# Kernel optimization log

Hardware: AMD Instinct MI355X
Metric: run time of the kernel (lower is better)

Reference implementation:

```python
import jax, jax.numpy as jnp
import numpy as np

C = 256
HEADS = 8
HD = C // HEADS
SCALE = HD ** -0.5


def conv1x1(x, W, b):
    # x: [B,C_in,H,W], W: [C_out,C_in], b: [C_out]
    return jnp.einsum('oc,bchw->bohw', W, x) + b[None, :, None, None]


def setup_inputs() -> dict:
    key = jax.random.key(0)
    ks = jax.random.split(key, 12)
    B, H, Wd = 2, 48, 48
    s = C ** -0.5
    return {
        'x': jax.random.normal(ks[0], (B, C, H, Wd), jnp.float32),
        'uncertainty': jax.random.uniform(ks[1], (B, 1, H, Wd), jnp.float32),
        'Wq': jax.random.normal(ks[2], (C, C), jnp.float32) * s,
        'bq': jnp.zeros((C,), jnp.float32),
        'Wk': jax.random.normal(ks[3], (C, C), jnp.float32) * s,
        'bk': jnp.zeros((C,), jnp.float32),
        'Wv': jax.random.normal(ks[4], (C, C), jnp.float32) * s,
        'bv': jnp.zeros((C,), jnp.float32),
        'Wg': jax.random.normal(ks[5], (C, 1), jnp.float32),
        'bg': jnp.zeros((C,), jnp.float32),
        'Wo': jax.random.normal(ks[6], (C, C), jnp.float32) * s,
        'bo': jnp.zeros((C,), jnp.float32),
    }


def reference(x, uncertainty, Wq, bq, Wk, bk, Wv, bv, Wg, bg, Wo, bo):
    B, _, H, Wd = x.shape
    N = H * Wd
    # uncertainty gate (1x1 conv from 1 channel to C channels)
    uw = conv1x1(uncertainty, Wg, bg)            # [B,C,H,W]
    gated_x = x * (1.0 - uw)
    q = conv1x1(gated_x, Wq, bq).reshape(B, HEADS, HD, N)
    k = conv1x1(gated_x, Wk, bk).reshape(B, HEADS, HD, N)
    v = conv1x1(x, Wv, bv).reshape(B, HEADS, HD, N)
    # scores: [B,h,N,N] (query tokens n, key tokens m)
    scores = jnp.einsum('bhdn,bhdm->bhnm', q, k) * SCALE
    u_flat = uncertainty.reshape(B, 1, 1, N)      # mask over key axis
    scores = scores * (1.0 - u_flat)
    attn = jax.nn.softmax(scores, axis=-1)
    out = jnp.einsum('bhnm,bhdm->bhdn', attn, v)  # [B,h,hd,N]
    out = out.reshape(B, C, H, Wd)
    out = conv1x1(out, Wo, bo)
    return out + x
```

## Files before the change

kernel.cpp:

```cpp
#include <hip/hip_runtime.h>
#include <hip/hip_bf16.h>

typedef float f32x4 __attribute__((ext_vector_type(4)));
typedef __bf16 bf16x8 __attribute__((ext_vector_type(8)));
typedef __bf16 bf16x4 __attribute__((ext_vector_type(4)));
typedef short s16x4 __attribute__((ext_vector_type(4)));

constexpr int C = 256;
constexpr int N = 2304;
constexpr int T = 2 * N;

#if __has_builtin(__builtin_amdgcn_exp2f)
#define EXP2F(x) __builtin_amdgcn_exp2f(x)
#else
#define EXP2F(x) exp2f(x)
#endif

__device__ __forceinline__ bf16x8 load_bf8(const __bf16* p) {
    return *reinterpret_cast<const bf16x8*>(p);
}

__device__ __forceinline__ f32x4 mfma32(bf16x8 a, bf16x8 b, f32x4 c) {
    return __builtin_amdgcn_mfma_f32_16x16x32_bf16(a, b, c, 0, 0, 0);
}

#if __has_builtin(__builtin_amdgcn_mfma_f32_16x16x16bf16_1k)
__device__ __forceinline__ f32x4 mfma16(bf16x4 a, bf16x4 b, f32x4 c) {
    return __builtin_amdgcn_mfma_f32_16x16x16bf16_1k(
        __builtin_bit_cast(s16x4, a), __builtin_bit_cast(s16x4, b), c, 0, 0, 0);
}
#else
__device__ __forceinline__ f32x4 mfma16(bf16x4 a, bf16x4 b, f32x4 c) {
    f32x4 d;
    asm volatile("v_mfma_f32_16x16x16_bf16 %0, %1, %2, %3"
                 : "=v"(d) : "v"(a), "v"(b), "v"(c));
    return d;
}
#endif

__device__ __forceinline__ void gload_lds16(const __bf16* g, __bf16* l) {
    __builtin_amdgcn_global_load_lds(
        (const __attribute__((address_space(1))) void*)g,
        (__attribute__((address_space(3))) void*)l, 16, 0, 0);
}

#define VMCNT2() asm volatile("s_waitcnt vmcnt(2)" ::: "memory")
#define VMCNT0() asm volatile("s_waitcnt vmcnt(0)" ::: "memory")
#define LGKM0()  asm volatile("s_waitcnt lgkmcnt(0)" ::: "memory")

__global__ void prep_kernel(const float* __restrict__ x, const float* __restrict__ u,
                            const float* __restrict__ Wg, const float* __restrict__ bg,
                            const float* __restrict__ Wq, const float* __restrict__ Wk,
                            const float* __restrict__ Wv, const float* __restrict__ Wo,
                            __bf16* __restrict__ xT, __bf16* __restrict__ gxT,
                            __bf16* __restrict__ Wb) {
    __shared__ float tile[32][65];
    int t = threadIdx.x;
    if (blockIdx.x >= 576) {
        int u2 = blockIdx.x - 576;
        const float* srcs[4] = {Wq, Wk, Wv, Wo};
        int m = u2 >> 6;
        int idx = (u2 & 63) * 256 + t;
        float4 v = reinterpret_cast<const float4*>(srcs[m])[idx];
        bf16x4 o = { (__bf16)v.x, (__bf16)v.y, (__bf16)v.z, (__bf16)v.w };
        reinterpret_cast<bf16x4*>(Wb + m * 65536)[idx] = o;
        return;
    }
    int uu = blockIdx.x;
    int n0 = (uu % 36) * 64;
    int c0 = ((uu / 36) & 7) * 32;
    int b = uu / 288;
    const float* xp = x + (b * C + c0) * N + n0;
    #pragma unroll
    for (int rr = 0; rr < 8; ++rr) {
        int cl = rr * 4 + (t >> 6);
        int nl = t & 63;
        tile[cl][nl] = xp[cl * N + nl];
    }
    __syncthreads();
    int cq = (t & 7) * 4;
    #pragma unroll
    for (int it = 0; it < 2; ++it) {
        int nl = it * 32 + (t >> 3);
        float uv = u[b * N + n0 + nl];
        bf16x4 xo, go;
        #pragma unroll
        for (int jj = 0; jj < 4; ++jj) {
            int cch = c0 + cq + jj;
            float xv = tile[cq + jj][nl];
            float gate = 1.0f - (Wg[cch] * uv + bg[cch]);
            xo[jj] = (__bf16)xv;
            go[jj] = (__bf16)(xv * gate);
        }
        int tok = b * N + n0 + nl;
        *reinterpret_cast<bf16x4*>(xT + (long)tok * C + c0 + cq) = xo;
        *reinterpret_cast<bf16x4*>(gxT + (long)tok * C + c0 + cq) = go;
    }
}

__global__ __launch_bounds__(256) void qkv_kernel(const __bf16* __restrict__ Wb,
    const __bf16* __restrict__ xT, const __bf16* __restrict__ gxT,
    const float* __restrict__ bq, const float* __restrict__ bk, const float* __restrict__ bv,
    const float* __restrict__ u,
    __bf16* __restrict__ Q, __bf16* __restrict__ K, __bf16* __restrict__ V) {
    int L = blockIdx.x;
    int h = L & 7;
    int rest = L >> 3;
    int c = rest % 36;
    int z = rest / 36;
    int wave = threadIdx.x >> 6, lane = threadIdx.x & 63;
    int g = lane >> 4, r = lane & 15;
    int ow = h * 32 + (wave & 1) * 16;
    int t0 = c * 128 + (wave >> 1) * 64;
    const __bf16* W = Wb + z * 65536;
    const __bf16* inp = (z == 2) ? xT : gxT;
    f32x4 acc[4] = {};
    for (int k = 0; k < 8; ++k) {
        bf16x8 a = load_bf8(W + (ow + r) * C + k * 32 + g * 8);
        #pragma unroll
        for (int tb = 0; tb < 4; ++tb) {
            bf16x8 bfr = load_bf8(inp + (long)(t0 + tb * 16 + r) * C + k * 32 + g * 8);
            acc[tb] = mfma32(a, bfr, acc[tb]);
        }
    }
    const float* bias = (z == 0) ? bq : (z == 1) ? bk : bv;
    float bvw[4];
    #pragma unroll
    for (int i = 0; i < 4; ++i) bvw[i] = bias[ow + g * 4 + i];
    int d0 = (wave & 1) * 16 + g * 4;
    const float SC = 0.17677669529663687f * 1.4426950408889634f;
    #pragma unroll
    for (int tb = 0; tb < 4; ++tb) {
        int t = t0 + tb * 16 + r;
        int b = t / N, n = t % N;
        if (z == 2) {
            #pragma unroll
            for (int i = 0; i < 4; ++i)
                V[((long)(b * 8 + h) * 32 + d0 + i) * N + n] = (__bf16)(acc[tb][i] + bvw[i]);
        } else {
            bf16x4 outv;
            if (z == 1) {
                float scale = SC * (1.0f - u[t]);
                #pragma unroll
                for (int i = 0; i < 4; ++i) outv[i] = (__bf16)((acc[tb][i] + bvw[i]) * scale);
            } else {
                #pragma unroll
                for (int i = 0; i < 4; ++i) outv[i] = (__bf16)(acc[tb][i] + bvw[i]);
            }
            __bf16* dst = (z == 0) ? Q : K;
            *reinterpret_cast<bf16x4*>(dst + ((long)(b * 8 + h) * N + n) * 32 + d0) = outv;
        }
    }
}

__global__ __launch_bounds__(512) void attn_kernel(const __bf16* __restrict__ Q,
    const __bf16* __restrict__ K, const __bf16* __restrict__ V,
    __bf16* __restrict__ aoT) {
    __shared__ __bf16 sMem[16384];
    int id = blockIdx.x;
    int xcd = id & 7, j = id >> 3;
    int bh = xcd + 8 * (j / 36);
    int qblk = j % 36;
    int tid = threadIdx.x;
    int wave = tid >> 6, lane = tid & 63;
    int grp = wave >> 2, wv = wave & 3;
    int g = lane >> 4, r = lane & 15;
    int q0w = qblk * 64 + wv * 16;
    const __bf16* Qg = Q + (long)bh * N * 32;
    const __bf16* Kg = K + (long)bh * N * 32 + (long)grp * 1152 * 32;
    const __bf16* Vg = V + (long)bh * 32 * N + grp * 1152;
    bf16x8 qf = load_bf8(Qg + (q0w + r) * 32 + g * 8);
    int s_ = (wv << 6) | lane;
    int l_ = s_ ^ ((s_ >> 3) & 7);
    const __bf16* kS = Kg + (l_ >> 2) * 32 + (l_ & 3) * 8;
    const __bf16* vS = Vg + (long)(l_ >> 3) * N + (l_ & 7) * 8;
    __bf16* kB = sMem + grp * 8192;
    __bf16* vB = kB + 4096;
    int so = wv * 512;
    auto STAGE = [&](long m0, int buf) {
        gload_lds16(kS + m0 * 32, kB + buf * 2048 + so);
        gload_lds16(vS + m0,      vB + buf * 2048 + so);
    };
    int pk[4], pv[4][2];
    #pragma unroll
    for (int t = 0; t < 4; ++t) {
        int ck = (t * 16 + r) * 4 + g;
        pk[t] = (ck ^ ((ck >> 3) & 7)) * 8;
        #pragma unroll
        for (int dt = 0; dt < 2; ++dt) {
            int cv = (dt * 16 + r) * 8 + t * 2 + (g >> 1);
            pv[t][dt] = (cv ^ ((cv >> 3) & 7)) * 8 + (g & 1) * 4;
        }
    }
    bf16x4 onesv;
    #pragma unroll
    for (int i = 0; i < 4; ++i) onesv[i] = (__bf16)1.0f;
    f32x4 oa0 = {}, oa1 = {}, oal = {};
    STAGE(0, 0);
    STAGE(64, 1);
    for (int t = 0; t < 18; ++t) {
        if (t < 17) { VMCNT2(); } else { VMCNT0(); }
        __builtin_amdgcn_s_barrier();
        const __bf16* kb = kB + (t & 1) * 2048;
        const __bf16* vb = vB + (t & 1) * 2048;
        bf16x8 kc0 = load_bf8(kb + pk[0]);
        bf16x8 kc1 = load_bf8(kb + pk[1]);
        bf16x8 kc2 = load_bf8(kb + pk[2]);
        bf16x8 kc3 = load_bf8(kb + pk[3]);
        bf16x4 vf[4][2];
        #pragma unroll
        for (int tt = 0; tt < 4; ++tt)
            #pragma unroll
            for (int dt = 0; dt < 2; ++dt)
                vf[tt][dt] = *reinterpret_cast<const bf16x4*>(vb + pv[tt][dt]);
        f32x4 z = {};
        __builtin_amdgcn_s_setprio(1);
        f32x4 s0 = mfma32(kc0, qf, z);
        f32x4 s1 = mfma32(kc1, qf, z);
        f32x4 s2 = mfma32(kc2, qf, z);
        f32x4 s3 = mfma32(kc3, qf, z);
        __builtin_amdgcn_s_setprio(0);
        bf16x4 pa0, pa1, pa2, pa3;
        #pragma unroll
        for (int i = 0; i < 4; ++i) pa0[i] = (__bf16)EXP2F(s0[i]);
        #pragma unroll
        for (int i = 0; i < 4; ++i) pa1[i] = (__bf16)EXP2F(s1[i]);
        #pragma unroll
        for (int i = 0; i < 4; ++i) pa2[i] = (__bf16)EXP2F(s2[i]);
        #pragma unroll
        for (int i = 0; i < 4; ++i) pa3[i] = (__bf16)EXP2F(s3[i]);
        __builtin_amdgcn_s_setprio(1);
        oa0 = mfma16(vf[0][0], pa0, oa0);
        oa1 = mfma16(vf[0][1], pa0, oa1);
        oal = mfma16(onesv,    pa0, oal);
        oa0 = mfma16(vf[1][0], pa1, oa0);
        oa1 = mfma16(vf[1][1], pa1, oa1);
        oal = mfma16(onesv,    pa1, oal);
        oa0 = mfma16(vf[2][0], pa2, oa0);
        oa1 = mfma16(vf[2][1], pa2, oa1);
        oal = mfma16(onesv,    pa2, oal);
        oa0 = mfma16(vf[3][0], pa3, oa0);
        oa1 = mfma16(vf[3][1], pa3, oa1);
        oal = mfma16(onesv,    pa3, oal);
        __builtin_amdgcn_s_setprio(0);
        LGKM0();
        __builtin_amdgcn_s_barrier();
        if (t < 16)
            STAGE((long)(t + 2) * 64, t & 1);
    }
    __syncthreads();
    float* F = reinterpret_cast<float*>(sMem);
    float* D = F + 4096;
    int fb = (grp * 4 + wv) * 512 + r * 32;
    int sg = g ^ (r & 7);
    *reinterpret_cast<f32x4*>(F + fb + sg * 4) = oa0;
    *reinterpret_cast<f32x4*>(F + fb + (sg ^ 4) * 4) = oa1;
    if (g == 0) D[grp * 64 + wv * 16 + r] = oal[0];
    __syncthreads();
    {
        int q = tid >> 3;
        int dg = tid & 7;
        int qw = q >> 4, qq = q & 15;
        int off = qw * 512 + qq * 32 + ((dg ^ (qq & 7)) * 4);
        f32x4 sum = *reinterpret_cast<const f32x4*>(F + off) +
                    *reinterpret_cast<const f32x4*>(F + 2048 + off);
        float l = D[qw * 16 + qq] + D[64 + qw * 16 + qq];
        float inv = 1.0f / l;
        bf16x4 ov;
        #pragma unroll
        for (int i = 0; i < 4; ++i) ov[i] = (__bf16)(sum[i] * inv);
        int b = bh >> 3, h = bh & 7;
        *reinterpret_cast<bf16x4*>(
            aoT + (long)(b * N + qblk * 64 + q) * C + h * 32 + dg * 4) = ov;
    }
}

__global__ __launch_bounds__(256) void outp_kernel(const __bf16* __restrict__ Wb,
    const __bf16* __restrict__ aoT, const float* __restrict__ bo,
    const float* __restrict__ x, float* __restrict__ out) {
    int o0 = blockIdx.y * 64;
    int t0 = blockIdx.x * 16;
    int wave = threadIdx.x >> 6, lane = threadIdx.x & 63;
    int g = lane >> 4, r = lane & 15;
    int ow = o0 + wave * 16;
    const __bf16* W = Wb + 3 * 65536;
    f32x4 acc = {};
    for (int k = 0; k < 8; ++k) {
        bf16x8 a = load_bf8(W + (ow + r) * C + k * 32 + g * 8);
        bf16x8 bfr = load_bf8(aoT + (long)(t0 + r) * C + k * 32 + g * 8);
        acc = mfma32(a, bfr, acc);
    }
    float bvw[4];
    #pragma unroll
    for (int i = 0; i < 4; ++i) bvw[i] = bo[ow + g * 4 + i];
    int t = t0 + r;
    int b = t / N, n = t % N;
    #pragma unroll
    for (int i = 0; i < 4; ++i) {
        long idx = ((long)b * C + ow + g * 4 + i) * N + n;
        out[idx] = acc[i] + bvw[i] + x[idx];
    }
}

extern "C" void kernel_launch(void* const* d_in, const int* in_sizes, int n_in,
                              void* d_out, int out_size, void* d_ws, size_t ws_size,
                              hipStream_t stream) {
    const float* x  = (const float*)d_in[0];
    const float* u  = (const float*)d_in[1];
    const float* Wq = (const float*)d_in[2];
    const float* bq = (const float*)d_in[3];
    const float* Wk = (const float*)d_in[4];
    const float* bk = (const float*)d_in[5];
    const float* Wv = (const float*)d_in[6];
    const float* bv = (const float*)d_in[7];
    const float* Wg = (const float*)d_in[8];
    const float* bg = (const float*)d_in[9];
    const float* Wo = (const float*)d_in[10];
    const float* bo = (const float*)d_in[11];
    float* out = (float*)d_out;

    char* ws = (char*)d_ws;
    size_t off = 0;
    auto alloc = [&](size_t bytes) {
        char* p = ws + off;
        off += (bytes + 255) & ~(size_t)255;
        return p;
    };
    __bf16* Wb  = (__bf16*)alloc((size_t)4 * 65536 * 2);
    __bf16* xT  = (__bf16*)alloc((size_t)T * C * 2);
    __bf16* gxT = (__bf16*)alloc((size_t)T * C * 2);
    __bf16* Qb  = (__bf16*)alloc((size_t)16 * N * 32 * 2);
    __bf16* Kb  = (__bf16*)alloc((size_t)16 * N * 32 * 2);
    __bf16* Vb  = (__bf16*)alloc((size_t)16 * N * 32 * 2);
    __bf16* aoT = (__bf16*)alloc((size_t)T * C * 2);

    prep_kernel<<<832, 256, 0, stream>>>(x, u, Wg, bg, Wq, Wk, Wv, Wo, xT, gxT, Wb);
    qkv_kernel<<<864, 256, 0, stream>>>(Wb, xT, gxT, bq, bk, bv, u, Qb, Kb, Vb);
    attn_kernel<<<576, 512, 0, stream>>>(Qb, Kb, Vb, aoT);
    outp_kernel<<<dim3(288, 4), 256, 0, stream>>>(Wb, aoT, bo, x, out);
}
```

Measured before the change: 68.57 us.

## Process two query tiles per wave in attention to reuse staged K/V

Each attention block now covers 128 queries instead of 64, with every wave holding two Q fragments and running the score and PV MFMAs for both against the same K/V tiles in shared memory. This halves global K/V staging traffic and barrier overhead per query, and halves the grid to 288 blocks. In exchange it uses more registers and a larger epilogue reduction buffer. With 288 blocks on 256 CUs the last wave of blocks is poorly balanced.

```diff
diff --git a/kernel.cpp b/kernel.cpp
--- a/kernel.cpp
+++ b/kernel.cpp
@@ -156,20 +156,21 @@
 __global__ __launch_bounds__(512) void attn_kernel(const __bf16* __restrict__ Q,
     const __bf16* __restrict__ K, const __bf16* __restrict__ V,
     __bf16* __restrict__ aoT) {
-    __shared__ __bf16 sMem[16384];
+    __shared__ __bf16 sMem[16896];
     int id = blockIdx.x;
     int xcd = id & 7, j = id >> 3;
-    int bh = xcd + 8 * (j / 36);
-    int qblk = j % 36;
+    int bh = xcd + 8 * (j / 18);
+    int qblk = j % 18;
     int tid = threadIdx.x;
     int wave = tid >> 6, lane = tid & 63;
     int grp = wave >> 2, wv = wave & 3;
     int g = lane >> 4, r = lane & 15;
-    int q0w = qblk * 64 + wv * 16;
+    int qbase = qblk * 128;
     const __bf16* Qg = Q + (long)bh * N * 32;
     const __bf16* Kg = K + (long)bh * N * 32 + (long)grp * 1152 * 32;
     const __bf16* Vg = V + (long)bh * 32 * N + grp * 1152;
-    bf16x8 qf = load_bf8(Qg + (q0w + r) * 32 + g * 8);
+    bf16x8 qf0 = load_bf8(Qg + (qbase + wv * 16 + r) * 32 + g * 8);
+    bf16x8 qf1 = load_bf8(Qg + (qbase + 64 + wv * 16 + r) * 32 + g * 8);
     int s_ = (wv << 6) | lane;
     int l_ = s_ ^ ((s_ >> 3) & 7);
     const __bf16* kS = Kg + (l_ >> 2) * 32 + (l_ & 3) * 8;
@@ -195,7 +196,8 @@
     bf16x4 onesv;
     #pragma unroll
     for (int i = 0; i < 4; ++i) onesv[i] = (__bf16)1.0f;
-    f32x4 oa0 = {}, oa1 = {}, oal = {};
+    f32x4 oa00 = {}, oa01 = {}, oa10 = {}, oa11 = {};
+    f32x4 oal0 = {}, oal1 = {};
     STAGE(0, 0);
     STAGE(64, 1);
     for (int t = 0; t < 18; ++t) {
@@ -215,33 +217,57 @@
                 vf[tt][dt] = *reinterpret_cast<const bf16x4*>(vb + pv[tt][dt]);
         f32x4 z = {};
         __builtin_amdgcn_s_setprio(1);
-        f32x4 s0 = mfma32(kc0, qf, z);
-        f32x4 s1 = mfma32(kc1, qf, z);
-        f32x4 s2 = mfma32(kc2, qf, z);
-        f32x4 s3 = mfma32(kc3, qf, z);
+        f32x4 sa0 = mfma32(kc0, qf0, z);
+        f32x4 sa1 = mfma32(kc1, qf0, z);
+        f32x4 sa2 = mfma32(kc2, qf0, z);
+        f32x4 sa3 = mfma32(kc3, qf0, z);
+        f32x4 sb0 = mfma32(kc0, qf1, z);
+        f32x4 sb1 = mfma32(kc1, qf1, z);
+        f32x4 sb2 = mfma32(kc2, qf1, z);
+        f32x4 sb3 = mfma32(kc3, qf1, z);
         __builtin_amdgcn_s_setprio(0);
-        bf16x4 pa0, pa1, pa2, pa3;
-        #pragma unroll
-        for (int i = 0; i < 4; ++i) pa0[i] = (__bf16)EXP2F(s0[i]);
-        #pragma unroll
-        for (int i = 0; i < 4; ++i) pa1[i] = (__bf16)EXP2F(s1[i]);
-        #pragma unroll
-        for (int i = 0; i < 4; ++i) pa2[i] = (__bf16)EXP2F(s2[i]);
-        #pragma unroll
-        for (int i = 0; i < 4; ++i) pa3[i] = (__bf16)EXP2F(s3[i]);
+        bf16x4 pa0, pa1, pa2, pa3, pb0, pb1, pb2, pb3;
+        #pragma unroll
+        for (int i = 0; i < 4; ++i) pa0[i] = (__bf16)EXP2F(sa0[i]);
+        #pragma unroll
+        for (int i = 0; i < 4; ++i) pa1[i] = (__bf16)EXP2F(sa1[i]);
+        #pragma unroll
+        for (int i = 0; i < 4; ++i) pa2[i] = (__bf16)EXP2F(sa2[i]);
+        #pragma unroll
+        for (int i = 0; i < 4; ++i) pa3[i] = (__bf16)EXP2F(sa3[i]);
+        #pragma unroll
+        for (int i = 0; i < 4; ++i) pb0[i] = (__bf16)EXP2F(sb0[i]);
+        #pragma unroll
+        for (int i = 0; i < 4; ++i) pb1[i] = (__bf16)EXP2F(sb1[i]);
+        #pragma unroll
+        for (int i = 0; i < 4; ++i) pb2[i] = (__bf16)EXP2F(sb2[i]);
+        #pragma unroll
+        for (int i = 0; i < 4; ++i) pb3[i] = (__bf16)EXP2F(sb3[i]);
         __builtin_amdgcn_s_setprio(1);
-        oa0 = mfma16(vf[0][0], pa0, oa0);
-        oa1 = mfma16(vf[0][1], pa0, oa1);
-        oal = mfma16(onesv,    pa0, oal);
-        oa0 = mfma16(vf[1][0], pa1, oa0);
-        oa1 = mfma16(vf[1][1], pa1, oa1);
-        oal = mfma16(onesv,    pa1, oal);
-        oa0 = mfma16(vf[2][0], pa2, oa0);
-        oa1 = mfma16(vf[2][1], pa2, oa1);
-        oal = mfma16(onesv,    pa2, oal);
-        oa0 = mfma16(vf[3][0], pa3, oa0);
-        oa1 = mfma16(vf[3][1], pa3, oa1);
-        oal = mfma16(onesv,    pa3, oal);
+        oa00 = mfma16(vf[0][0], pa0, oa00);
+        oa01 = mfma16(vf[0][1], pa0, oa01);
+        oal0 = mfma16(onesv,    pa0, oal0);
+        oa10 = mfma16(vf[0][0], pb0, oa10);
+        oa11 = mfma16(vf[0][1], pb0, oa11);
+        oal1 = mfma16(onesv,    pb0, oal1);
+        oa00 = mfma16(vf[1][0], pa1, oa00);
+        oa01 = mfma16(vf[1][1], pa1, oa01);
+        oal0 = mfma16(onesv,    pa1, oal0);
+        oa10 = mfma16(vf[1][0], pb1, oa10);
+        oa11 = mfma16(vf[1][1], pb1, oa11);
+        oal1 = mfma16(onesv,    pb1, oal1);
+        oa00 = mfma16(vf[2][0], pa2, oa00);
+        oa01 = mfma16(vf[2][1], pa2, oa01);
+        oal0 = mfma16(onesv,    pa2, oal0);
+        oa10 = mfma16(vf[2][0], pb2, oa10);
+        oa11 = mfma16(vf[2][1], pb2, oa11);
+        oal1 = mfma16(onesv,    pb2, oal1);
+        oa00 = mfma16(vf[3][0], pa3, oa00);
+        oa01 = mfma16(vf[3][1], pa3, oa01);
+        oal0 = mfma16(onesv,    pa3, oal0);
+        oa10 = mfma16(vf[3][0], pb3, oa10);
+        oa11 = mfma16(vf[3][1], pb3, oa11);
+        oal1 = mfma16(onesv,    pb3, oal1);
         __builtin_amdgcn_s_setprio(0);
         LGKM0();
         __builtin_amdgcn_s_barrier();
@@ -250,28 +276,35 @@
     }
     __syncthreads();
     float* F = reinterpret_cast<float*>(sMem);
-    float* D = F + 4096;
-    int fb = (grp * 4 + wv) * 512 + r * 32;
+    float* D = F + 8192;
+    int fb = (grp * 4 + wv) * 1024 + r * 32;
     int sg = g ^ (r & 7);
-    *reinterpret_cast<f32x4*>(F + fb + sg * 4) = oa0;
-    *reinterpret_cast<f32x4*>(F + fb + (sg ^ 4) * 4) = oa1;
-    if (g == 0) D[grp * 64 + wv * 16 + r] = oal[0];
+    *reinterpret_cast<f32x4*>(F + fb + sg * 4) = oa00;
+    *reinterpret_cast<f32x4*>(F + fb + (sg ^ 4) * 4) = oa01;
+    *reinterpret_cast<f32x4*>(F + fb + 512 + sg * 4) = oa10;
+    *reinterpret_cast<f32x4*>(F + fb + 512 + (sg ^ 4) * 4) = oa11;
+    if (g == 0) {
+        D[(grp * 4 + wv) * 32 + r] = oal0[0];
+        D[(grp * 4 + wv) * 32 + 16 + r] = oal1[0];
+    }
     __syncthreads();
-    {
-        int q = tid >> 3;
-        int dg = tid & 7;
-        int qw = q >> 4, qq = q & 15;
-        int off = qw * 512 + qq * 32 + ((dg ^ (qq & 7)) * 4);
+    int b = bh >> 3, h = bh & 7;
+    #pragma unroll
+    for (int k2 = 0; k2 < 2; ++k2) {
+        int uidx = tid + k2 * 512;
+        int q = uidx >> 3;
+        int dg = uidx & 7;
+        int qt = q >> 6, wvq = (q >> 4) & 3, qq = q & 15;
+        int off = wvq * 1024 + qt * 512 + qq * 32 + ((dg ^ (qq & 7)) * 4);
         f32x4 sum = *reinterpret_cast<const f32x4*>(F + off) +
-                    *reinterpret_cast<const f32x4*>(F + 2048 + off);
-        float l = D[qw * 16 + qq] + D[64 + qw * 16 + qq];
+                    *reinterpret_cast<const f32x4*>(F + 4096 + off);
+        float l = D[wvq * 32 + qt * 16 + qq] + D[128 + wvq * 32 + qt * 16 + qq];
         float inv = 1.0f / l;
         bf16x4 ov;
         #pragma unroll
         for (int i = 0; i < 4; ++i) ov[i] = (__bf16)(sum[i] * inv);
-        int b = bh >> 3, h = bh & 7;
         *reinterpret_cast<bf16x4*>(
-            aoT + (long)(b * N + qblk * 64 + q) * C + h * 32 + dg * 4) = ov;
+            aoT + (long)(b * N + qbase + q) * C + h * 32 + dg * 4) = ov;
     }
 }
 
@@ -336,6 +369,6 @@
 
     prep_kernel<<<832, 256, 0, stream>>>(x, u, Wg, bg, Wq, Wk, Wv, Wo, xT, gxT, Wb);
     qkv_kernel<<<864, 256, 0, stream>>>(Wb, xT, gxT, bq, bk, bv, u, Qb, Kb, Vb);
-    attn_kernel<<<576, 512, 0, stream>>>(Qb, Kb, Vb, aoT);
+    attn_kernel<<<288, 512, 0, stream>>>(Qb, Kb, Vb, aoT);
     outp_kernel<<<dim3(288, 4), 256, 0, stream>>>(Wb, aoT, bo, x, out);
 }
```

Measured after the change: 75.22 us. 1.1x slower.
